# Kernel tuning notes

Measured on AMD Instinct MI355X. Metric: run time of the kernel, lower is better.

## Reference

```python
import jax, jax.numpy as jnp
import numpy as np

B, S, D, H, NUM_LABELS = 16, 1024, 1024, 16, 3
LN_EPS = 1e-5


def setup_inputs() -> dict:
    key = jax.random.key(0)
    ks = iter(jax.random.split(key, 16))

    def w(shape, k):
        return jax.random.normal(k, shape, jnp.float32) * 0.02

    inp = {}
    inp["embedded"] = jax.random.normal(next(ks), (B, S, D), jnp.float32)
    inp["attention_mask"] = jnp.ones((B, S), jnp.float32)
    for pfx in ("p2h", "h2p"):
        for name in ("q", "k", "v", "o"):
            inp[f"{pfx}_W{name}"] = w((D, D), next(ks))
            inp[f"{pfx}_b{name}"] = jnp.zeros((D,), jnp.float32)
        inp[f"{pfx}_ln_g"] = jnp.ones((D,), jnp.float32)
        inp[f"{pfx}_ln_b"] = jnp.zeros((D,), jnp.float32)
    inp["W1"] = w((4 * D, D), next(ks)); inp["b1"] = jnp.zeros((D,), jnp.float32)
    inp["W2"] = w((D, D // 2), next(ks)); inp["b2"] = jnp.zeros((D // 2,), jnp.float32)
    inp["W3"] = w((D // 2, NUM_LABELS), next(ks)); inp["b3"] = jnp.zeros((NUM_LABELS,), jnp.float32)
    return inp


def _layernorm(x, g, b):
    mu = jnp.mean(x, axis=-1, keepdims=True)
    var = jnp.mean(jnp.square(x - mu), axis=-1, keepdims=True)
    return (x - mu) / jnp.sqrt(var + LN_EPS) * g + b


def _cross_attn(q_in, kv_in, kv_mask, Wq, bq, Wk, bk, Wv, bv, Wo, bo, g, bln):
    Bs, Sq, Dm = q_in.shape
    Sk = kv_in.shape[1]
    hd = Dm // H
    Q = (q_in @ Wq + bq).reshape(Bs, Sq, H, hd)
    K = (kv_in @ Wk + bk).reshape(Bs, Sk, H, hd)
    V = (kv_in @ Wv + bv).reshape(Bs, Sk, H, hd)
    scores = jnp.einsum("bqhd,bkhd->bhqk", Q, K) / jnp.sqrt(jnp.float32(hd))
    scores = jnp.where(kv_mask[:, None, None, :] == 0, jnp.float32(-1e9), scores)
    wts = jax.nn.softmax(scores, axis=-1)  # dropout is identity in eval
    att = jnp.einsum("bhqk,bkhd->bqhd", wts, V).reshape(Bs, Sq, Dm)
    return _layernorm(att @ Wo + bo + q_in, g, bln)


def _pool(x, m):
    s = jnp.sum(x * m[:, :, None], axis=1)
    d = jnp.clip(jnp.sum(m, axis=1, keepdims=True), 1e-9, None)
    return s / d


def reference(embedded, attention_mask,
              p2h_Wq, p2h_bq, p2h_Wk, p2h_bk, p2h_Wv, p2h_bv, p2h_Wo, p2h_bo, p2h_ln_g, p2h_ln_b,
              h2p_Wq, h2p_bq, h2p_Wk, h2p_bk, h2p_Wv, h2p_bv, h2p_Wo, h2p_bo, h2p_ln_g, h2p_ln_b,
              W1, b1, W2, b2, W3, b3):
    half = embedded.shape[1] // 2
    premise, hypothesis = embedded[:, :half], embedded[:, half:]
    pm, hm = attention_mask[:, :half], attention_mask[:, half:]
    p2h = _cross_attn(premise, hypothesis, hm,
                      p2h_Wq, p2h_bq, p2h_Wk, p2h_bk, p2h_Wv, p2h_bv, p2h_Wo, p2h_bo, p2h_ln_g, p2h_ln_b)
    h2p = _cross_attn(hypothesis, premise, pm,
                      h2p_Wq, h2p_bq, h2p_Wk, h2p_bk, h2p_Wv, h2p_bv, h2p_Wo, h2p_bo, h2p_ln_g, h2p_ln_b)
    feats = jnp.concatenate([_pool(premise, pm), _pool(hypothesis, hm),
                             _pool(p2h, pm), _pool(h2p, hm)], axis=-1)
    h1 = jax.nn.relu(feats @ W1 + b1)
    h2 = jax.nn.relu(h1 @ W2 + b2)
    return h2 @ W3 + b3
```

## Files before the change

kernel.cpp:

```cpp
#include <hip/hip_runtime.h>
#include <hip/hip_bf16.h>

typedef __attribute__((ext_vector_type(8))) __bf16 bf16x8;
typedef __attribute__((ext_vector_type(4))) float f32x4;
typedef __attribute__((ext_vector_type(4))) int i32x4;
typedef __attribute__((ext_vector_type(4))) unsigned short u16x4;

#define MFMA16(a, b, c) __builtin_amdgcn_mfma_f32_16x16x32_bf16((a), (b), (c), 0, 0, 0)

__device__ __forceinline__ void gload_lds16(const void* g, void* l)
{
    __builtin_amdgcn_global_load_lds(
        (const __attribute__((address_space(1))) unsigned int*)g,
        (__attribute__((address_space(3))) unsigned int*)l, 16, 0, 0);
}

struct GemmW { const __bf16* w[2]; const float* bias[2]; const float* bias2[2]; };
struct LnW   { const float* g[2]; const float* b[2]; };

__global__ __launch_bounds__(256) void cast_emb_kernel(const float* __restrict__ emb,
                                                       __bf16* __restrict__ A)
{
    int i = (blockIdx.x * 256 + threadIdx.x) * 4;
    int r = i >> 10, d = i & 1023;
    size_t src = ((size_t)(r >> 9) * 1024 + (r & 511)) * 1024 + d;
    f32x4 p = *(const f32x4*)(emb + src);
    f32x4 h = *(const f32x4*)(emb + src + 512 * 1024);
    union { __bf16 b[4]; u16x4 u; } cp, ch;
#pragma unroll
    for (int j = 0; j < 4; ++j) { cp.b[j] = (__bf16)p[j]; ch.b[j] = (__bf16)h[j]; }
    *(u16x4*)(A + i) = cp.u;
    *(u16x4*)(A + 8388608 + i) = ch.u;
}

struct WPtrs { const float* p[8]; };
__global__ __launch_bounds__(256) void cast_wt_kernel(WPtrs wp, __bf16* __restrict__ Wt0)
{
    const float* W = wp.p[blockIdx.z];
    __bf16* Wt = Wt0 + (size_t)blockIdx.z * 1048576;
    __shared__ float tile[32][33];
    int n0 = blockIdx.x * 32, k0 = blockIdx.y * 32;
    int tx = threadIdx.x, ty = threadIdx.y;
#pragma unroll
    for (int i = ty; i < 32; i += 8)
        tile[i][tx] = W[(size_t)(k0 + i) * 1024 + n0 + tx];
    __syncthreads();
#pragma unroll
    for (int i = ty; i < 32; i += 8)
        Wt[(size_t)(n0 + i) * 1024 + k0 + tx] = (__bf16)tile[tx][i];
}

template <int EPI>
__global__ __launch_bounds__(256, 3) void gemm_bt(const __bf16* __restrict__ A,
                                                  GemmW gw,
                                                  __bf16* __restrict__ Cb,
                                                  __bf16* __restrict__ Vt,
                                                  float* __restrict__ Cf,
                                                  const float* __restrict__ resid,
                                                  int K)
{
    __shared__ __align__(16) __bf16 As[128 * 32];
    __shared__ __align__(16) __bf16 Bs[128 * 32];
    const int t = threadIdx.x;
    const int l = t & 63, w = t >> 6;
    const int wr = w >> 1, wc = w & 1;
    const int lrow = l & 15, lk = l >> 4;
    const int m0 = blockIdx.y * 128, n0 = blockIdx.x * 128;
    const int dir = m0 >> 13;
    const int r0 = t >> 2, kc0 = (t & 3) * 8;

    const int am0 = (EPI == 3) ? (m0 ^ 8192) : m0;
    const __bf16* Bt = gw.w[dir];
    const __bf16* gA0 = A + (size_t)(am0 + r0) * K + kc0;
    const __bf16* gA1 = gA0 + (size_t)64 * K;
    const __bf16* gB0 = Bt + (size_t)(n0 + r0) * K + kc0;
    const __bf16* gB1 = gB0 + (size_t)64 * K;
    __bf16* dA0 = &As[r0 * 32 + kc0];
    __bf16* dA1 = &As[(r0 + 64) * 32 + kc0];
    __bf16* dB0 = &Bs[r0 * 32 + kc0];
    __bf16* dB1 = &Bs[(r0 + 64) * 32 + kc0];

    const f32x4 zero = {0.f, 0.f, 0.f, 0.f};
    f32x4 acc[4][4];
#pragma unroll
    for (int mi = 0; mi < 4; ++mi)
#pragma unroll
        for (int ni = 0; ni < 4; ++ni) acc[mi][ni] = zero;

    const int nk = K >> 5;
    for (int kt = 0; kt < nk; ++kt) {
        const int ko = kt * 32;
        gload_lds16(gA0 + ko, dA0);
        gload_lds16(gA1 + ko, dA1);
        gload_lds16(gB0 + ko, dB0);
        gload_lds16(gB1 + ko, dB1);
        __syncthreads();
        bf16x8 af[4], bfv[4];
#pragma unroll
        for (int mi = 0; mi < 4; ++mi)
            af[mi] = *(const bf16x8*)(&As[(wr * 64 + mi * 16 + lrow) * 32 + lk * 8]);
#pragma unroll
        for (int ni = 0; ni < 4; ++ni)
            bfv[ni] = *(const bf16x8*)(&Bs[(wc * 64 + ni * 16 + lrow) * 32 + lk * 8]);
#pragma unroll
        for (int mi = 0; mi < 4; ++mi)
#pragma unroll
            for (int ni = 0; ni < 4; ++ni)
                acc[mi][ni] = MFMA16(af[mi], bfv[ni], acc[mi][ni]);
        __syncthreads();
    }

#pragma unroll
    for (int mi = 0; mi < 4; ++mi) {
#pragma unroll
        for (int ni = 0; ni < 4; ++ni) {
            int col = n0 + wc * 64 + ni * 16 + lrow;
            float bv = (EPI == 3 && col >= 1024) ? gw.bias2[dir][col - 1024]
                                                 : gw.bias[dir][col & 1023];
#pragma unroll
            for (int r = 0; r < 4; ++r) {
                int row = m0 + wr * 64 + mi * 16 + lk * 4 + r;
                float v = acc[mi][ni][r] + bv;
                if (EPI == 0) {
                    Cb[(size_t)row * 1024 + col] = (__bf16)v;
                } else if (EPI == 3) {
                    if (col < 1024) {
                        Cb[(size_t)row * 1024 + col] = (__bf16)v;
                    } else {
                        int c2 = col - 1024;
                        int local = row & 8191;
                        int b_ = local >> 9, pos = local & 511;
                        int h_ = c2 >> 6, hd = c2 & 63;
                        Vt[(size_t)dir * 8388608 +
                           (((size_t)(b_ * 16 + h_) * 64 + hd) << 9) + pos] = (__bf16)v;
                    }
                } else {
                    int local = row & 8191;
                    int b_ = local >> 9, s = local & 511;
                    int rh = dir * 512;
                    float rv = resid[((size_t)b_ * 1024 + rh + s) * 1024 + col];
                    Cf[(size_t)row * 1024 + col] = v + rv;
                }
            }
        }
    }
}

__global__ __launch_bounds__(256, 3) void attn_kernel(const __bf16* __restrict__ Q,
                                                      const __bf16* __restrict__ Kb,
                                                      const __bf16* __restrict__ Vt,
                                                      const float* __restrict__ mask,
                                                      __bf16* __restrict__ att)
{
    __shared__ __align__(16) __bf16 KB[2][128 * 64];
    __shared__ __align__(16) __bf16 Pt[64 * 128];
    __shared__ __align__(16) float msk[512];
    const int dirbh = blockIdx.x;
    const int dir = dirbh >> 8, bh = dirbh & 255;
    const int b = bh >> 4, h = bh & 15;
    const int mask_half = dir ? 0 : 512;
    const int q0 = blockIdx.y * 64;
    const int tid = threadIdx.x, l = tid & 63, w = tid >> 6;
    const int lrow = l & 15, lk = l >> 4;
    const size_t rowbase = (size_t)dir * 8192 + b * 512;

    const __bf16* kbase = Kb + rowbase * 1024 + h * 64;
    const __bf16* vsrc = Vt + (size_t)dir * 8388608 + (size_t)bh * 64 * 512;

    auto stage = [&](int t, int buf) {
        char* dst = (char*)KB[buf];
#pragma unroll
        for (int i = 0; i < 4; ++i) {
            int c = tid + i * 256;
            int pos = c >> 3, gslot = (c & 7) ^ (pos & 7);
            gload_lds16(kbase + (size_t)(t * 128 + pos) * 1024 + gslot * 8, dst + c * 16);
        }
    };

    stage(0, 0);
    for (int i = tid; i < 512; i += 256) msk[i] = mask[b * 1024 + mask_half + i];

    const __bf16* qptr = Q + (rowbase + q0 + w * 16 + lrow) * 1024 + h * 64;
    bf16x8 qf0 = *(const bf16x8*)(qptr + lk * 8);
    bf16x8 qf1 = *(const bf16x8*)(qptr + 32 + lk * 8);

    const f32x4 zero = {0.f, 0.f, 0.f, 0.f};
    f32x4 av[4];
#pragma unroll
    for (int ni = 0; ni < 4; ++ni) av[ni] = zero;
    float m_run = -3e38f, su = 0.f;
    const int psw = lrow & 7;
    char* prowp = (char*)Pt + (w * 16 + lrow) * 256;
    f32x4 sc[8];

#pragma unroll
    for (int t = 0; t < 4; ++t) {
        __syncthreads();
        const char* kbuf = (const char*)KB[t & 1];
#pragma unroll
        for (int jj = 0; jj < 8; ++jj) {
            const char* kb = kbuf + (jj * 16 + lrow) * 128;
            bf16x8 k0 = *(const bf16x8*)(kb + ((lk ^ psw) << 4));
            bf16x8 k1 = *(const bf16x8*)(kb + (((lk + 4) ^ psw) << 4));
            f32x4 c = zero;
            c = MFMA16(k0, qf0, c);
            c = MFMA16(k1, qf1, c);
            sc[jj] = c;
        }
        if (t < 3) stage(t + 1, (t + 1) & 1);

        const int koff = t * 128;
        float mt = -3e38f;
#pragma unroll
        for (int jj = 0; jj < 8; ++jj) {
            f32x4 mv = *(const f32x4*)(&msk[koff + jj * 16 + lk * 4]);
#pragma unroll
            for (int r = 0; r < 4; ++r) {
                float s = sc[jj][r] * 0.125f;
                if (mv[r] == 0.f) s = -1e9f;
                sc[jj][r] = s;
                mt = fmaxf(mt, s);
            }
        }
        mt = fmaxf(mt, __shfl_xor(mt, 16));
        mt = fmaxf(mt, __shfl_xor(mt, 32));
        float m_new = fmaxf(m_run, mt);
        float f = __expf(m_run - m_new);
        float s0 = 0.f, s1 = 0.f;
#pragma unroll
        for (int jj = 0; jj < 8; ++jj) {
            float e0 = __expf(sc[jj][0] - m_new);
            float e1 = __expf(sc[jj][1] - m_new);
            float e2 = __expf(sc[jj][2] - m_new);
            float e3 = __expf(sc[jj][3] - m_new);
            sc[jj][0] = e0; sc[jj][1] = e1; sc[jj][2] = e2; sc[jj][3] = e3;
            s0 += e0 + e1;
            s1 += e2 + e3;
        }
        float ssum = s0 + s1;
        ssum += __shfl_xor(ssum, 16);
        ssum += __shfl_xor(ssum, 32);
        su = su * f + ssum;
        m_run = m_new;
#pragma unroll
        for (int r = 0; r < 4; ++r) {
            float fr = __shfl(f, (l & 48) | (lk * 4 + r));
#pragma unroll
            for (int ni = 0; ni < 4; ++ni) av[ni][r] *= fr;
        }

#pragma unroll
        for (int jj = 0; jj < 8; ++jj) {
            union { __bf16 b[4]; unsigned long long u; } pk;
#pragma unroll
            for (int r = 0; r < 4; ++r) pk.b[r] = (__bf16)sc[jj][r];
            int slot2 = jj * 2 + (lk >> 1);
            *(unsigned long long*)(prowp + (((slot2 ^ psw) << 4) | ((lk & 1) << 3))) = pk.u;
        }
#pragma unroll
        for (int ks = 0; ks < 4; ++ks) {
            bf16x8 pf = *(const bf16x8*)(prowp + (((ks * 4 + lk) ^ psw) << 4));
#pragma unroll
            for (int ni = 0; ni < 4; ++ni) {
                bf16x8 vf = *(const bf16x8*)(&vsrc[(ni * 16 + lrow) * 512 + koff + ks * 32 + lk * 8]);
                av[ni] = MFMA16(pf, vf, av[ni]);
            }
        }
    }

    const float inv = 1.f / su;
#pragma unroll
    for (int r = 0; r < 4; ++r) {
        float ivr = __shfl(inv, (l & 48) | (lk * 4 + r));
        size_t orow = rowbase + q0 + w * 16 + lk * 4 + r;
#pragma unroll
        for (int ni = 0; ni < 4; ++ni)
            att[orow * 1024 + h * 64 + ni * 16 + lrow] = (__bf16)(av[ni][r] * ivr);
    }
}

__global__ __launch_bounds__(256) void ln_kernel(const float* __restrict__ X,
                                                 LnW lw,
                                                 __bf16* __restrict__ out)
{
    const int r = blockIdx.x, t = threadIdx.x;
    const int dir = r >> 13;
    const float* g = lw.g[dir];
    const float* bta = lw.b[dir];
    const float* x = X + (size_t)r * 1024;
    f32x4 v = *(const f32x4*)(x + t * 4);
    float s = v[0] + v[1] + v[2] + v[3];
    float q = v[0] * v[0] + v[1] * v[1] + v[2] * v[2] + v[3] * v[3];
#pragma unroll
    for (int d = 1; d < 64; d <<= 1) { s += __shfl_xor(s, d); q += __shfl_xor(q, d); }
    __shared__ float rs[4], rq[4];
    if ((t & 63) == 0) { rs[t >> 6] = s; rq[t >> 6] = q; }
    __syncthreads();
    s = rs[0] + rs[1] + rs[2] + rs[3];
    q = rq[0] + rq[1] + rq[2] + rq[3];
    float mu = s * (1.f / 1024.f);
    float var = q * (1.f / 1024.f) - mu * mu;
    float rstd = rsqrtf(var + 1e-5f);
#pragma unroll
    for (int j = 0; j < 4; ++j) {
        int c = t * 4 + j;
        out[(size_t)r * 1024 + c] = (__bf16)((v[j] - mu) * rstd * g[c] + bta[c]);
    }
}

__global__ __launch_bounds__(256) void pool_f32_kernel(const float* __restrict__ X,
                                                       const float* __restrict__ mask,
                                                       float* __restrict__ feats)
{
    const int b = blockIdx.y, d0 = blockIdx.x * 64, half = blockIdx.z * 512;
    const int t = threadIdx.x, d = d0 + (t & 63), sl = t >> 6;
    float acc = 0.f, ms = 0.f;
#pragma unroll 4
    for (int s = sl * 128; s < sl * 128 + 128; ++s) {
        float m = mask[b * 1024 + half + s];
        acc += X[((size_t)b * 1024 + half + s) * 1024 + d] * m;
        ms += m;
    }
    __shared__ float ra[4][64];
    __shared__ float rm[4];
    ra[sl][t & 63] = acc;
    if ((t & 63) == 0) rm[sl] = ms;
    __syncthreads();
    if (t < 64) {
        float a = ra[0][t] + ra[1][t] + ra[2][t] + ra[3][t];
        float m = rm[0] + rm[1] + rm[2] + rm[3];
        feats[b * 4096 + blockIdx.z * 1024 + d0 + t] = a / fmaxf(m, 1e-9f);
    }
}

__global__ __launch_bounds__(256) void pool_bf16_kernel(const __bf16* __restrict__ X,
                                                        const float* __restrict__ mask,
                                                        float* __restrict__ feats)
{
    const int b = blockIdx.y, d0 = blockIdx.x * 64, dir = blockIdx.z;
    const int half = dir * 512;
    const int t = threadIdx.x, d = d0 + (t & 63), sl = t >> 6;
    float acc = 0.f, ms = 0.f;
#pragma unroll 4
    for (int s = sl * 128; s < sl * 128 + 128; ++s) {
        float m = mask[b * 1024 + half + s];
        acc += (float)X[((size_t)dir * 8192 + b * 512 + s) * 1024 + d] * m;
        ms += m;
    }
    __shared__ float ra[4][64];
    __shared__ float rm[4];
    ra[sl][t & 63] = acc;
    if ((t & 63) == 0) rm[sl] = ms;
    __syncthreads();
    if (t < 64) {
        float a = ra[0][t] + ra[1][t] + ra[2][t] + ra[3][t];
        float m = rm[0] + rm[1] + rm[2] + rm[3];
        feats[b * 4096 + 2048 + dir * 1024 + d0 + t] = a / fmaxf(m, 1e-9f);
    }
}

__global__ __launch_bounds__(256) void fc_init_kernel(const float* __restrict__ b1,
                                                      const float* __restrict__ b2,
                                                      float* __restrict__ h1,
                                                      float* __restrict__ h2)
{
    int i = blockIdx.x * 256 + threadIdx.x;
    if (i < 16 * 1024) h1[i] = b1[i & 1023];
    else h2[i - 16 * 1024] = b2[(i - 16 * 1024) & 511];
}

template <int CH, int RELU_IN>
__global__ __launch_bounds__(256) void fc_atomic_kernel(const float* __restrict__ in,
                                                        const float* __restrict__ W,
                                                        float* __restrict__ out,
                                                        int IF, int OF)
{
    __shared__ float ins[16 * CH];
    const int t = threadIdx.x;
    const int col = blockIdx.x * 256 + t;
    const int i0 = blockIdx.y * CH;
#pragma unroll
    for (int idx = t; idx < 16 * CH; idx += 256) {
        int b = idx / CH, i = idx % CH;
        float v = in[b * IF + i0 + i];
        if (RELU_IN) v = fmaxf(v, 0.f);
        ins[idx] = v;
    }
    __syncthreads();
    float acc[16];
#pragma unroll
    for (int b = 0; b < 16; ++b) acc[b] = 0.f;
#pragma unroll 4
    for (int i = 0; i < CH; ++i) {
        float wv = W[(size_t)(i0 + i) * OF + col];
#pragma unroll
        for (int b = 0; b < 16; ++b) acc[b] += ins[b * CH + i] * wv;
    }
#pragma unroll
    for (int b = 0; b < 16; ++b) atomicAdd(out + b * OF + col, acc[b]);
}

__global__ __launch_bounds__(64) void mlp3_kernel(const float* __restrict__ h2,
                                                  const float* __restrict__ W3,
                                                  const float* __restrict__ b3,
                                                  float* __restrict__ out)
{
    int b = blockIdx.x, t = threadIdx.x;
    float a0 = 0.f, a1 = 0.f, a2 = 0.f;
    for (int i = t; i < 512; i += 64) {
        float hv = fmaxf(h2[b * 512 + i], 0.f);
        a0 += hv * W3[i * 3 + 0];
        a1 += hv * W3[i * 3 + 1];
        a2 += hv * W3[i * 3 + 2];
    }
#pragma unroll
    for (int d = 1; d < 64; d <<= 1) {
        a0 += __shfl_xor(a0, d);
        a1 += __shfl_xor(a1, d);
        a2 += __shfl_xor(a2, d);
    }
    if (t == 0) {
        out[b * 3 + 0] = a0 + b3[0];
        out[b * 3 + 1] = a1 + b3[1];
        out[b * 3 + 2] = a2 + b3[2];
    }
}

extern "C" void kernel_launch(void* const* d_in, const int* in_sizes, int n_in,
                              void* d_out, int out_size, void* d_ws, size_t ws_size,
                              hipStream_t stream)
{
    const float* emb  = (const float*)d_in[0];
    const float* mask = (const float*)d_in[1];
    const float* W1 = (const float*)d_in[22];
    const float* b1 = (const float*)d_in[23];
    const float* W2 = (const float*)d_in[24];
    const float* b2 = (const float*)d_in[25];
    const float* W3 = (const float*)d_in[26];
    const float* b3 = (const float*)d_in[27];

    char* ws = (char*)d_ws;
    constexpr size_t MB = 1ull << 20;
    __bf16* A     = (__bf16*)(ws);
    __bf16* Wt    = (__bf16*)(ws + 32 * MB);
    __bf16* Qb    = (__bf16*)(ws + 48 * MB);
    __bf16* Kb    = (__bf16*)(ws + 80 * MB);
    __bf16* Vt    = (__bf16*)(ws + 112 * MB);
    __bf16* attb  = (__bf16*)(ws);
    float*  Of    = (float*) (ws + 48 * MB);
    __bf16* ctx   = (__bf16*)(ws);
    float*  feats = (float*) (ws + 144 * MB);
    float*  h1    = (float*) (ws + 144 * MB + 512 * 1024);
    float*  h2    = (float*) (ws + 145 * MB);

    cast_emb_kernel<<<8192, 256, 0, stream>>>(emb, A);
    WPtrs wp;
    const int widx[8] = {2, 4, 6, 8, 12, 14, 16, 18};
    for (int i = 0; i < 8; ++i) wp.p[i] = (const float*)d_in[widx[i]];
    cast_wt_kernel<<<dim3(32, 32, 8), dim3(32, 8), 0, stream>>>(wp, Wt);

    GemmW gq, gkv, go;
    LnW lw;
    for (int dir = 0; dir < 2; ++dir) {
        const int base = dir ? 12 : 2;
        gq.w[dir]  = Wt + (size_t)(dir * 4 + 0) * 1048576;
        gq.bias[dir]  = (const float*)d_in[base + 1];
        gq.bias2[dir] = nullptr;
        gkv.w[dir] = Wt + (size_t)(dir * 4 + 1) * 1048576;
        gkv.bias[dir]  = (const float*)d_in[base + 3];
        gkv.bias2[dir] = (const float*)d_in[base + 5];
        go.w[dir]  = Wt + (size_t)(dir * 4 + 3) * 1048576;
        go.bias[dir]  = (const float*)d_in[base + 7];
        go.bias2[dir] = nullptr;
        lw.g[dir] = (const float*)d_in[base + 8];
        lw.b[dir] = (const float*)d_in[base + 9];
    }

    gemm_bt<0><<<dim3(8, 128), 256, 0, stream>>>(A, gq, Qb, nullptr, nullptr, nullptr, 1024);
    gemm_bt<3><<<dim3(16, 128), 256, 0, stream>>>(A, gkv, Kb, Vt, nullptr, nullptr, 1024);
    attn_kernel<<<dim3(512, 8), 256, 0, stream>>>(Qb, Kb, Vt, mask, attb);
    gemm_bt<2><<<dim3(8, 128), 256, 0, stream>>>(attb, go, nullptr, nullptr, Of, emb, 1024);
    ln_kernel<<<16384, 256, 0, stream>>>(Of, lw, ctx);
    pool_bf16_kernel<<<dim3(16, 16, 2), 256, 0, stream>>>(ctx, mask, feats);
    pool_f32_kernel<<<dim3(16, 16, 2), 256, 0, stream>>>(emb, mask, feats);

    fc_init_kernel<<<96, 256, 0, stream>>>(b1, b2, h1, h2);
    fc_atomic_kernel<128, 0><<<dim3(4, 32), 256, 0, stream>>>(feats, W1, h1, 4096, 1024);
    fc_atomic_kernel<32, 1><<<dim3(2, 32), 256, 0, stream>>>(h1, W2, h2, 1024, 512);
    mlp3_kernel<<<16, 64, 0, stream>>>(h2, W3, b3, (float*)d_out);
}
```

Before: 569.2 us.

## Merge Q/K/V projections into one GEMM, fold LayerNorm into pooling, hoist V fragments

Combines the separate Q and K/V projection GEMMs into one launch with a 24-column-tile grid, where the segment index picks the bias, the A-half and the output layout. The LayerNorm kernel now writes only per-row mean and rstd. Pooling reads the fp32 pre-norm output and applies normalisation and the gain/bias algebraically, which drops the bf16 context write and read. In attention, V fragments are loaded into registers before the softmax step instead of inside the PV MFMA loop, which raises register pressure.

```diff
diff --git a/kernel.cpp b/kernel.cpp
--- a/kernel.cpp
+++ b/kernel.cpp
@@ -15,8 +15,7 @@
         (__attribute__((address_space(3))) unsigned int*)l, 16, 0, 0);
 }
 
-struct GemmW { const __bf16* w[2]; const float* bias[2]; const float* bias2[2]; };
-struct LnW   { const float* g[2]; const float* b[2]; };
+struct LnW { const float* g[2]; const float* b[2]; };
 
 __global__ __launch_bounds__(256) void cast_emb_kernel(const float* __restrict__ emb,
                                                        __bf16* __restrict__ A)
@@ -50,14 +49,14 @@
         Wt[(size_t)(n0 + i) * 1024 + k0 + tx] = (__bf16)tile[tx][i];
 }
 
+struct GArgs {
+    const __bf16* w[2];
+    const float* bias[6];
+    __bf16* Qb; __bf16* Kb; __bf16* Vt;
+    float* Cf; const float* resid;
+};
 template <int EPI>
-__global__ __launch_bounds__(256, 3) void gemm_bt(const __bf16* __restrict__ A,
-                                                  GemmW gw,
-                                                  __bf16* __restrict__ Cb,
-                                                  __bf16* __restrict__ Vt,
-                                                  float* __restrict__ Cf,
-                                                  const float* __restrict__ resid,
-                                                  int K)
+__global__ __launch_bounds__(256, 3) void gemm_bt(const __bf16* __restrict__ A, GArgs a)
 {
     __shared__ __align__(16) __bf16 As[128 * 32];
     __shared__ __align__(16) __bf16 Bs[128 * 32];
@@ -67,10 +66,12 @@
     const int lrow = l & 15, lk = l >> 4;
     const int m0 = blockIdx.y * 128, n0 = blockIdx.x * 128;
     const int dir = m0 >> 13;
+    const int seg = (EPI == 5) ? (n0 >> 10) : 0;
     const int r0 = t >> 2, kc0 = (t & 3) * 8;
-
-    const int am0 = (EPI == 3) ? (m0 ^ 8192) : m0;
-    const __bf16* Bt = gw.w[dir];
+    const int K = 1024;
+
+    const int am0 = (EPI == 5 && seg != 0) ? (m0 ^ 8192) : m0;
+    const __bf16* Bt = a.w[dir];
     const __bf16* gA0 = A + (size_t)(am0 + r0) * K + kc0;
     const __bf16* gA1 = gA0 + (size_t)64 * K;
     const __bf16* gB0 = Bt + (size_t)(n0 + r0) * K + kc0;
@@ -87,8 +88,7 @@
 #pragma unroll
         for (int ni = 0; ni < 4; ++ni) acc[mi][ni] = zero;
 
-    const int nk = K >> 5;
-    for (int kt = 0; kt < nk; ++kt) {
+    for (int kt = 0; kt < 32; ++kt) {
         const int ko = kt * 32;
         gload_lds16(gA0 + ko, dA0);
         gload_lds16(gA1 + ko, dA1);
@@ -110,36 +110,35 @@
         __syncthreads();
     }
 
+    const float* bsel = a.bias[dir * 3 + seg];
 #pragma unroll
     for (int mi = 0; mi < 4; ++mi) {
 #pragma unroll
         for (int ni = 0; ni < 4; ++ni) {
             int col = n0 + wc * 64 + ni * 16 + lrow;
-            float bv = (EPI == 3 && col >= 1024) ? gw.bias2[dir][col - 1024]
-                                                 : gw.bias[dir][col & 1023];
+            int c2 = col & 1023;
+            float bv = bsel[c2];
 #pragma unroll
             for (int r = 0; r < 4; ++r) {
                 int row = m0 + wr * 64 + mi * 16 + lk * 4 + r;
                 float v = acc[mi][ni][r] + bv;
-                if (EPI == 0) {
-                    Cb[(size_t)row * 1024 + col] = (__bf16)v;
-                } else if (EPI == 3) {
-                    if (col < 1024) {
-                        Cb[(size_t)row * 1024 + col] = (__bf16)v;
+                if (EPI == 5) {
+                    if (seg == 0) {
+                        a.Qb[(size_t)row * 1024 + c2] = (__bf16)v;
+                    } else if (seg == 1) {
+                        a.Kb[(size_t)row * 1024 + c2] = (__bf16)v;
                     } else {
-                        int c2 = col - 1024;
                         int local = row & 8191;
                         int b_ = local >> 9, pos = local & 511;
                         int h_ = c2 >> 6, hd = c2 & 63;
-                        Vt[(size_t)dir * 8388608 +
-                           (((size_t)(b_ * 16 + h_) * 64 + hd) << 9) + pos] = (__bf16)v;
+                        a.Vt[(size_t)dir * 8388608 +
+                             (((size_t)(b_ * 16 + h_) * 64 + hd) << 9) + pos] = (__bf16)v;
                     }
                 } else {
                     int local = row & 8191;
                     int b_ = local >> 9, s = local & 511;
-                    int rh = dir * 512;
-                    float rv = resid[((size_t)b_ * 1024 + rh + s) * 1024 + col];
-                    Cf[(size_t)row * 1024 + col] = v + rv;
+                    float rv = a.resid[((size_t)b_ * 1024 + dir * 512 + s) * 1024 + c2];
+                    a.Cf[(size_t)row * 1024 + c2] = v + rv;
                 }
             }
         }
@@ -192,6 +191,7 @@
     const int psw = lrow & 7;
     char* prowp = (char*)Pt + (w * 16 + lrow) * 256;
     f32x4 sc[8];
+    bf16x8 vfr[16];
 
 #pragma unroll
     for (int t = 0; t < 4; ++t) {
@@ -210,6 +210,13 @@
         if (t < 3) stage(t + 1, (t + 1) & 1);
 
         const int koff = t * 128;
+#pragma unroll
+        for (int ks = 0; ks < 4; ++ks)
+#pragma unroll
+            for (int ni = 0; ni < 4; ++ni)
+                vfr[ks * 4 + ni] =
+                    *(const bf16x8*)(&vsrc[(ni * 16 + lrow) * 512 + koff + ks * 32 + lk * 8]);
+
         float mt = -3e38f;
 #pragma unroll
         for (int jj = 0; jj < 8; ++jj) {
@@ -261,10 +268,8 @@
         for (int ks = 0; ks < 4; ++ks) {
             bf16x8 pf = *(const bf16x8*)(prowp + (((ks * 4 + lk) ^ psw) << 4));
 #pragma unroll
-            for (int ni = 0; ni < 4; ++ni) {
-                bf16x8 vf = *(const bf16x8*)(&vsrc[(ni * 16 + lrow) * 512 + koff + ks * 32 + lk * 8]);
-                av[ni] = MFMA16(pf, vf, av[ni]);
-            }
+            for (int ni = 0; ni < 4; ++ni)
+                av[ni] = MFMA16(pf, vfr[ks * 4 + ni], av[ni]);
         }
     }
 
@@ -279,14 +284,10 @@
     }
 }
 
-__global__ __launch_bounds__(256) void ln_kernel(const float* __restrict__ X,
-                                                 LnW lw,
-                                                 __bf16* __restrict__ out)
+__global__ __launch_bounds__(256) void ln_stats_kernel(const float* __restrict__ X,
+                                                       float2* __restrict__ stats)
 {
     const int r = blockIdx.x, t = threadIdx.x;
-    const int dir = r >> 13;
-    const float* g = lw.g[dir];
-    const float* bta = lw.b[dir];
     const float* x = X + (size_t)r * 1024;
     f32x4 v = *(const f32x4*)(x + t * 4);
     float s = v[0] + v[1] + v[2] + v[3];
@@ -296,15 +297,12 @@
     __shared__ float rs[4], rq[4];
     if ((t & 63) == 0) { rs[t >> 6] = s; rq[t >> 6] = q; }
     __syncthreads();
-    s = rs[0] + rs[1] + rs[2] + rs[3];
-    q = rq[0] + rq[1] + rq[2] + rq[3];
-    float mu = s * (1.f / 1024.f);
-    float var = q * (1.f / 1024.f) - mu * mu;
-    float rstd = rsqrtf(var + 1e-5f);
-#pragma unroll
-    for (int j = 0; j < 4; ++j) {
-        int c = t * 4 + j;
-        out[(size_t)r * 1024 + c] = (__bf16)((v[j] - mu) * rstd * g[c] + bta[c]);
+    if (t == 0) {
+        s = rs[0] + rs[1] + rs[2] + rs[3];
+        q = rq[0] + rq[1] + rq[2] + rq[3];
+        float mu = s * (1.f / 1024.f);
+        float var = q * (1.f / 1024.f) - mu * mu;
+        stats[r] = make_float2(mu, rsqrtf(var + 1e-5f));
     }
 }
 
@@ -333,9 +331,11 @@
     }
 }
 
-__global__ __launch_bounds__(256) void pool_bf16_kernel(const __bf16* __restrict__ X,
-                                                        const float* __restrict__ mask,
-                                                        float* __restrict__ feats)
+__global__ __launch_bounds__(256) void pool_ln_kernel(const float* __restrict__ Of,
+                                                      const float2* __restrict__ stats,
+                                                      const float* __restrict__ mask,
+                                                      LnW lw,
+                                                      float* __restrict__ feats)
 {
     const int b = blockIdx.y, d0 = blockIdx.x * 64, dir = blockIdx.z;
     const int half = dir * 512;
@@ -344,7 +344,10 @@
 #pragma unroll 4
     for (int s = sl * 128; s < sl * 128 + 128; ++s) {
         float m = mask[b * 1024 + half + s];
-        acc += (float)X[((size_t)dir * 8192 + b * 512 + s) * 1024 + d] * m;
+        int row = dir * 8192 + b * 512 + s;
+        float2 st = stats[row];
+        float x = Of[(size_t)row * 1024 + d];
+        acc += m * (x - st.x) * st.y;
         ms += m;
     }
     __shared__ float ra[4][64];
@@ -355,7 +358,8 @@
     if (t < 64) {
         float a = ra[0][t] + ra[1][t] + ra[2][t] + ra[3][t];
         float m = rm[0] + rm[1] + rm[2] + rm[3];
-        feats[b * 4096 + 2048 + dir * 1024 + d0 + t] = a / fmaxf(m, 1e-9f);
+        float g = lw.g[dir][d0 + t], bb = lw.b[dir][d0 + t];
+        feats[b * 4096 + 2048 + dir * 1024 + d0 + t] = (g * a + bb * m) / fmaxf(m, 1e-9f);
     }
 }
 
@@ -448,10 +452,10 @@
     __bf16* Vt    = (__bf16*)(ws + 112 * MB);
     __bf16* attb  = (__bf16*)(ws);
     float*  Of    = (float*) (ws + 48 * MB);
-    __bf16* ctx   = (__bf16*)(ws);
     float*  feats = (float*) (ws + 144 * MB);
     float*  h1    = (float*) (ws + 144 * MB + 512 * 1024);
     float*  h2    = (float*) (ws + 145 * MB);
+    float2* stats = (float2*)(ws + 146 * MB);
 
     cast_emb_kernel<<<8192, 256, 0, stream>>>(emb, A);
     WPtrs wp;
@@ -459,29 +463,27 @@
     for (int i = 0; i < 8; ++i) wp.p[i] = (const float*)d_in[widx[i]];
     cast_wt_kernel<<<dim3(32, 32, 8), dim3(32, 8), 0, stream>>>(wp, Wt);
 
-    GemmW gq, gkv, go;
+    GArgs gqkv = {}, go = {};
     LnW lw;
     for (int dir = 0; dir < 2; ++dir) {
         const int base = dir ? 12 : 2;
-        gq.w[dir]  = Wt + (size_t)(dir * 4 + 0) * 1048576;
-        gq.bias[dir]  = (const float*)d_in[base + 1];
-        gq.bias2[dir] = nullptr;
-        gkv.w[dir] = Wt + (size_t)(dir * 4 + 1) * 1048576;
-        gkv.bias[dir]  = (const float*)d_in[base + 3];
-        gkv.bias2[dir] = (const float*)d_in[base + 5];
-        go.w[dir]  = Wt + (size_t)(dir * 4 + 3) * 1048576;
-        go.bias[dir]  = (const float*)d_in[base + 7];
-        go.bias2[dir] = nullptr;
+        gqkv.w[dir] = Wt + (size_t)(dir * 4) * 1048576;
+        gqkv.bias[dir * 3 + 0] = (const float*)d_in[base + 1];
+        gqkv.bias[dir * 3 + 1] = (const float*)d_in[base + 3];
+        gqkv.bias[dir * 3 + 2] = (const float*)d_in[base + 5];
+        go.w[dir] = Wt + (size_t)(dir * 4 + 3) * 1048576;
+        go.bias[dir * 3] = (const float*)d_in[base + 7];
         lw.g[dir] = (const float*)d_in[base + 8];
         lw.b[dir] = (const float*)d_in[base + 9];
     }
-
-    gemm_bt<0><<<dim3(8, 128), 256, 0, stream>>>(A, gq, Qb, nullptr, nullptr, nullptr, 1024);
-    gemm_bt<3><<<dim3(16, 128), 256, 0, stream>>>(A, gkv, Kb, Vt, nullptr, nullptr, 1024);
+    gqkv.Qb = Qb; gqkv.Kb = Kb; gqkv.Vt = Vt;
+    go.Cf = Of; go.resid = emb;
+
+    gemm_bt<5><<<dim3(24, 128), 256, 0, stream>>>(A, gqkv);
     attn_kernel<<<dim3(512, 8), 256, 0, stream>>>(Qb, Kb, Vt, mask, attb);
-    gemm_bt<2><<<dim3(8, 128), 256, 0, stream>>>(attb, go, nullptr, nullptr, Of, emb, 1024);
-    ln_kernel<<<16384, 256, 0, stream>>>(Of, lw, ctx);
-    pool_bf16_kernel<<<dim3(16, 16, 2), 256, 0, stream>>>(ctx, mask, feats);
+    gemm_bt<2><<<dim3(8, 128), 256, 0, stream>>>(attb, go);
+    ln_stats_kernel<<<16384, 256, 0, stream>>>(Of, stats);
+    pool_ln_kernel<<<dim3(16, 16, 2), 256, 0, stream>>>(Of, stats, mask, lw, feats);
     pool_f32_kernel<<<dim3(16, 16, 2), 256, 0, stream>>>(emb, mask, feats);
 
     fc_init_kernel<<<96, 256, 0, stream>>>(b1, b2, h1, h2);
```

Result: faster. 541.0 us (-5.0%).
